# Kernel tuning notes

Measured on AMD Instinct MI355X. Metric: run time of the kernel, lower is better.

## Reference

```python
import jax, jax.numpy as jnp
import numpy as np

B = 512        # batch
D = 128        # embedding_dim (n_input)
S = 50         # max_tweets_num (n_sequence)
T = 32         # max_seq_len (n_steps)
HOOPS = 2
NUM_USERS = 20000
NUM_ITEMS = 100000
LATENT = 64
NUM_FRIENDS = 10000
CLIP = 50      # friend_clip
PAD = 50000    # vocab.pad; word table has PAD+1 rows


def setup_inputs() -> dict:
    key = jax.random.key(0)
    ks = jax.random.split(key, 24)
    s = 0.02
    emb_word = (jax.random.normal(ks[0], (PAD + 1, D)) * s).at[PAD].set(0.0)
    emb_item = jax.random.normal(ks[1], (NUM_ITEMS, LATENT)) * s
    emb_user = (jax.random.normal(ks[2], (NUM_FRIENDS + 1, LATENT)) * s).at[NUM_FRIENDS].set(0.0)
    W_mem = jax.random.normal(ks[3], (LATENT, D)) * s
    b_mem = jnp.zeros((D,))
    w_word = jax.random.normal(ks[4], (D,)) * s
    b_word = jnp.zeros(())
    w_sent = jax.random.normal(ks[5], (D,)) * s
    b_sent = jnp.zeros(())
    W_tr = jax.random.normal(ks[6], (D, LATENT)) * s
    b_tr = jnp.zeros((LATENT,))
    W1 = jax.random.normal(ks[7], (LATENT, LATENT // 2)) * s
    b1 = jnp.zeros((LATENT // 2,))
    W2 = jax.random.normal(ks[8], (LATENT // 2, LATENT // 4)) * s
    b2 = jnp.zeros((LATENT // 4,))
    W3 = jax.random.normal(ks[9], (LATENT // 4, 2)) * s
    b3 = jnp.zeros((2,))
    w_aff = jax.random.normal(ks[10], (LATENT,)) * s
    b_aff = jnp.zeros(())
    user_tweet_indices = jax.random.randint(ks[11], (NUM_USERS, S, T), 0, PAD)
    ufi = jax.random.randint(ks[12], (NUM_USERS, CLIP), 0, NUM_FRIENDS)
    # simulate padded friend lists in the trailing slots
    user_friend_indices = ufi.at[:, CLIP - 5:].set(NUM_FRIENDS)
    user_indices = jax.random.randint(ks[13], (B,), 0, NUM_USERS)
    item_indices = jax.random.randint(ks[14], (B,), 0, NUM_ITEMS)
    return {
        'user_indices': user_indices, 'item_indices': item_indices,
        'emb_word': emb_word, 'emb_item': emb_item, 'emb_user': emb_user,
        'W_mem': W_mem, 'b_mem': b_mem, 'w_word': w_word, 'b_word': b_word,
        'w_sent': w_sent, 'b_sent': b_sent, 'W_tr': W_tr, 'b_tr': b_tr,
        'W1': W1, 'b1': b1, 'W2': W2, 'b2': b2, 'W3': W3, 'b3': b3,
        'w_aff': w_aff, 'b_aff': b_aff,
        'user_tweet_indices': user_tweet_indices,
        'user_friend_indices': user_friend_indices,
    }


def reference(user_indices, item_indices, emb_word, emb_item, emb_user,
              W_mem, b_mem, w_word, b_word, w_sent, b_sent, W_tr, b_tr,
              W1, b1, W2, b2, W3, b3, w_aff, b_aff,
              user_tweet_indices, user_friend_indices):
    item_emb = emb_item[item_indices]                       # [B, L]
    mem = item_emb @ W_mem + b_mem                          # [B, D]
    tweets = emb_word[user_tweet_indices[user_indices]]     # [B, S, T, D]
    for _ in range(HOOPS):
        # word-level attention: scores via broadcast mul+sum == einsum
        ww = jax.nn.softmax(jnp.einsum('bstd,bd->bst', tweets, mem), axis=2)
        sentence = jnp.einsum('bst,bstd->bsd', ww, tweets)  # [B, S, D]
        sw = sentence @ w_word + b_word                     # [B, S]
        iw = mem @ w_sent + b_sent                          # [B]
        swf = jax.nn.softmax(jnp.tanh(sw + iw[:, None]), axis=1)
        mem = jnp.einsum('bs,bsd->bd', swf, sentence) + mem
    ept = mem @ W_tr + b_tr                                 # [B, L]
    fidx = user_friend_indices[user_indices]                # [B, C]
    femb = emb_user[fidx]                                   # [B, C, L]
    friend_num = CLIP - (fidx == NUM_FRIENDS).sum(axis=1, keepdims=True).astype(jnp.float32)
    group_idx = jax.nn.sigmoid(
        jnp.einsum('bcl,l->bc', item_emb[:, None, :] * femb, w_aff) + b_aff)[..., None]
    femb = femb * group_idx
    user_emb = femb.sum(axis=1) / friend_num                # [B, L]
    a = jax.nn.sigmoid(item_emb @ W1 + b1)
    a = jax.nn.sigmoid(a @ W2 + b2)
    alpha = jax.nn.sigmoid(a @ W3 + b3)                     # [B, 2]
    vector = alpha[:, 0:1] * ept + alpha[:, 1:2] * user_emb
    rating = jax.nn.sigmoid((vector * item_emb) @ w_aff + b_aff)  # [B]
    return rating, group_idx
```

## Files before the change

kernel.cpp:

```cpp
#include <hip/hip_runtime.h>
#include <hip/hip_fp16.h>

#define NB 512
#define DD 128
#define SS 50
#define TT 32
#define LL 64
#define CLIPN 50
#define NFRIENDS 10000
#define NTHREADS 512
#define NWAVES 8
#define PAD1 50001
#define WELEMS (PAD1 * DD)

typedef unsigned short u16;
typedef unsigned int u32;

__device__ __forceinline__ float bf2f(u32 u) {
    union { u32 i; float f; } c; c.i = u << 16; return c.f;
}
__device__ __forceinline__ u16 f2bf(float f) {
    union { float f; u32 i; } c; c.f = f;
    u32 x = c.i;
    return (u16)((x + 0x7fffu + ((x >> 16) & 1u)) >> 16);
}
__device__ __forceinline__ float sigf(float x) { return 1.f / (1.f + expf(-x)); }

__device__ __forceinline__ void e5m2_dec4(u32 w, float* o) {
    union { u32 u; __half2 h; } lo, hi;
    lo.u = ((w & 0x000000ffu) << 8) | ((w & 0x0000ff00u) << 16);
    hi.u = ((w & 0x00ff0000u) >> 8) | (w & 0xff000000u);
    float2 a = __half22float2(lo.h), b = __half22float2(hi.h);
    o[0] = a.x; o[1] = a.y; o[2] = b.x; o[3] = b.y;
}
__device__ __forceinline__ u32 e5m2_byte(float x) {
    u16 h = __half_as_ushort(__float2half(x));
    u16 r = (u16)(h + 0x7Fu + ((h >> 8) & 1u));
    return (r >> 8) & 0xffu;
}
__device__ __forceinline__ u32 e5m2_enc4(const float* v) {
    return e5m2_byte(v[0]) | (e5m2_byte(v[1]) << 8) |
           (e5m2_byte(v[2]) << 16) | (e5m2_byte(v[3]) << 24);
}

template <bool BF16> struct LD;
template <> struct LD<true> {
    static __device__ __forceinline__ float one(const void* p, long i) {
        return bf2f(((const u16*)p)[i]);
    }
    static __device__ __forceinline__ void st(void* p, long i, float v) {
        ((u16*)p)[i] = f2bf(v);
    }
};
template <> struct LD<false> {
    static __device__ __forceinline__ float one(const void* p, long i) {
        return ((const float*)p)[i];
    }
    static __device__ __forceinline__ void st(void* p, long i, float v) {
        ((float*)p)[i] = v;
    }
};

template <int WM> struct WT;
template <> struct WT<0> {
    static __device__ __forceinline__ void sixteen(const void* p, long i, float* o) {
        const float* s = (const float*)p + i;
        #pragma unroll
        for (int j = 0; j < 4; ++j) {
            float4 v = *(const float4*)(s + 4 * j);
            o[4*j] = v.x; o[4*j+1] = v.y; o[4*j+2] = v.z; o[4*j+3] = v.w;
        }
    }
    static __device__ __forceinline__ void four(const void* p, long i, float* o) {
        float4 v = *(const float4*)((const float*)p + i);
        o[0] = v.x; o[1] = v.y; o[2] = v.z; o[3] = v.w;
    }
};
template <> struct WT<1> {
    static __device__ __forceinline__ void sixteen(const void* p, long i, float* o) {
        const u16* s = (const u16*)p + i;
        #pragma unroll
        for (int j = 0; j < 2; ++j) {
            uint4 v = *(const uint4*)(s + 8 * j);
            float* q = o + 8 * j;
            q[0] = bf2f(v.x & 0xffffu); q[1] = bf2f(v.x >> 16);
            q[2] = bf2f(v.y & 0xffffu); q[3] = bf2f(v.y >> 16);
            q[4] = bf2f(v.z & 0xffffu); q[5] = bf2f(v.z >> 16);
            q[6] = bf2f(v.w & 0xffffu); q[7] = bf2f(v.w >> 16);
        }
    }
    static __device__ __forceinline__ void four(const void* p, long i, float* o) {
        uint2 v = *(const uint2*)((const u16*)p + i);
        o[0] = bf2f(v.x & 0xffffu); o[1] = bf2f(v.x >> 16);
        o[2] = bf2f(v.y & 0xffffu); o[3] = bf2f(v.y >> 16);
    }
};
template <> struct WT<2> {
    static __device__ __forceinline__ void sixteen(const void* p, long i, float* o) {
        uint4 v = *(const uint4*)((const unsigned char*)p + i);
        e5m2_dec4(v.x, o); e5m2_dec4(v.y, o + 4);
        e5m2_dec4(v.z, o + 8); e5m2_dec4(v.w, o + 12);
    }
    static __device__ __forceinline__ void four(const void* p, long i, float* o) {
        e5m2_dec4(*(const u32*)((const unsigned char*)p + i), o);
    }
};

__global__ void sniff_dtype(const void* __restrict__ emb_word, int* __restrict__ flag) {
    const u16* p = (const u16*)emb_word;
    int lane = (int)threadIdx.x;
    int bad = 0;
    #pragma unroll
    for (int j = 0; j < 8; ++j) {
        unsigned e = (p[lane * 8 + j] >> 7) & 0xffu;
        bad += (e >= 127u);
    }
    #pragma unroll
    for (int off = 1; off < 64; off <<= 1) bad += __shfl_xor(bad, off, 64);
    if (lane == 0) flag[0] = (bad <= 16) ? 1 : 0;
}

__global__ void convert_words(const void* __restrict__ src, u32* __restrict__ dst,
                              const int* __restrict__ flag) {
    long idx = (long)blockIdx.x * 256 + threadIdx.x;
    long i = idx * 16;
    if (i >= WELEMS) return;
    float v[16];
    if (flag[0] == 0) {
        const float* s = (const float*)src + i;
        #pragma unroll
        for (int j = 0; j < 4; ++j) {
            float4 q = *(const float4*)(s + 4 * j);
            v[4*j] = q.x; v[4*j+1] = q.y; v[4*j+2] = q.z; v[4*j+3] = q.w;
        }
    } else {
        WT<1>::sixteen(src, i, v);
    }
    uint4 o;
    o.x = e5m2_enc4(v); o.y = e5m2_enc4(v + 4);
    o.z = e5m2_enc4(v + 8); o.w = e5m2_enc4(v + 12);
    *(uint4*)(dst + idx * 4) = o;
}

template <bool BF16, int WM>
__global__ __launch_bounds__(NTHREADS, 4)
void nrs_fused(const int* __restrict__ user_idx,
               const int* __restrict__ item_idx,
               const void* __restrict__ wtab,
               const void* __restrict__ emb_item,
               const void* __restrict__ emb_user,
               const void* __restrict__ W_mem, const void* __restrict__ b_mem,
               const void* __restrict__ w_word, const void* __restrict__ b_word,
               const void* __restrict__ w_sent, const void* __restrict__ b_sent,
               const void* __restrict__ W_tr, const void* __restrict__ b_tr,
               const void* __restrict__ W1, const void* __restrict__ b1,
               const void* __restrict__ W2, const void* __restrict__ b2,
               const void* __restrict__ W3, const void* __restrict__ b3,
               const void* __restrict__ w_aff, const void* __restrict__ b_aff,
               const int* __restrict__ uti, const int* __restrict__ ufi,
               void* __restrict__ out, const int* __restrict__ flag)
{
    if (flag[0] != (BF16 ? 1 : 0)) return;

    __shared__ float s_mem[DD];
    __shared__ float s_item[LL];
    __shared__ float s_sent[SS * DD];
    __shared__ int   s_uti[SS * TT];
    __shared__ float s_sw[SS];
    __shared__ float s_swf[SS];
    __shared__ float s_q[LL];
    __shared__ float s_ept[LL];
    __shared__ float s_uemb[LL];
    __shared__ int   s_fidx[CLIPN];
    __shared__ float s_g[CLIPN];
    __shared__ float s_a1[32];
    __shared__ float s_a2[16];
    __shared__ float s_alpha[2];
    __shared__ float s_fnum;

    const int b = blockIdx.x;
    const int tid = (int)threadIdx.x;
    const int lane = tid & 63;
    const int wave = tid >> 6;

    const int u = user_idx[b];
    const int it = item_idx[b];
    const long utb = (long)u * (SS * TT);

    if (tid < LL) s_item[tid] = LD<BF16>::one(emb_item, (long)it * LL + tid);
    __syncthreads();

    for (int i = tid; i < SS * TT; i += NTHREADS) s_uti[i] = uti[utb + i];
    if (tid < DD) {
        float acc = LD<BF16>::one(b_mem, tid);
        #pragma unroll 8
        for (int l = 0; l < LL; ++l)
            acc += s_item[l] * LD<BF16>::one(W_mem, l * DD + tid);
        s_mem[tid] = acc;
    }
    __syncthreads();

    const float bw = LD<BF16>::one(b_word, 0);
    const float bs = LD<BF16>::one(b_sent, 0);
    const int dq = lane & 31;
    const int th = lane >> 5;
    float ww4[4];
    #pragma unroll
    for (int k = 0; k < 4; ++k) ww4[k] = LD<BF16>::one(w_word, 4 * dq + k);
    const float ws0 = LD<BF16>::one(w_sent, lane);
    const float ws1 = LD<BF16>::one(w_sent, lane + 64);

    for (int hoop = 0; hoop < 2; ++hoop) {
        for (int s = wave; s < SS; s += NWAVES) {
            const int t = lane >> 1, h = lane & 1;
            const int row = s_uti[s * TT + t];
            const long base = (long)row * DD + h * 64;
            float acc = 0.f;
            #pragma unroll
            for (int j = 0; j < 4; ++j) {
                float v16[16];
                WT<WM>::sixteen(wtab, base + 16 * j, v16);
                const float* mp = &s_mem[h * 64 + 16 * j];
                #pragma unroll
                for (int k = 0; k < 16; ++k) acc += v16[k] * mp[k];
            }
            acc += __shfl_xor(acc, 1, 64);

            float mx = acc;
            #pragma unroll
            for (int off = 1; off < 64; off <<= 1) mx = fmaxf(mx, __shfl_xor(mx, off, 64));
            float e = expf(acc - mx);
            float sm = e;
            #pragma unroll
            for (int off = 1; off < 64; off <<= 1) sm += __shfl_xor(sm, off, 64);
            float wwt = 2.f * e / sm;

            float a4[4] = {0.f, 0.f, 0.f, 0.f};
            #pragma unroll 4
            for (int i2 = 0; i2 < 16; ++i2) {
                int t2 = th * 16 + i2;
                float wv = __shfl(wwt, 2 * t2, 64);
                int r2 = s_uti[s * TT + t2];
                float v4[4];
                WT<WM>::four(wtab, (long)r2 * DD + 4 * dq, v4);
                #pragma unroll
                for (int k = 0; k < 4; ++k) a4[k] += wv * v4[k];
            }
            #pragma unroll
            for (int k = 0; k < 4; ++k) a4[k] += __shfl_xor(a4[k], 32, 64);
            if (th == 0)
                *(float4*)&s_sent[s * DD + 4 * dq] =
                    make_float4(a4[0], a4[1], a4[2], a4[3]);

            float p = a4[0] * ww4[0] + a4[1] * ww4[1] + a4[2] * ww4[2] + a4[3] * ww4[3];
            #pragma unroll
            for (int off = 1; off < 64; off <<= 1) p += __shfl_xor(p, off, 64);
            if (lane == 0) s_sw[s] = 0.5f * p + bw;
        }
        __syncthreads();

        if (wave == 0) {
            float p = s_mem[lane] * ws0 + s_mem[lane + 64] * ws1;
            #pragma unroll
            for (int off = 1; off < 64; off <<= 1) p += __shfl_xor(p, off, 64);
            float iw = p + bs;
            float v = (lane < SS) ? tanhf(s_sw[lane] + iw) : -2.f;
            float mx = v;
            #pragma unroll
            for (int off = 1; off < 64; off <<= 1) mx = fmaxf(mx, __shfl_xor(mx, off, 64));
            float e = (lane < SS) ? expf(v - mx) : 0.f;
            float sm = e;
            #pragma unroll
            for (int off = 1; off < 64; off <<= 1) sm += __shfl_xor(sm, off, 64);
            if (lane < SS) s_swf[lane] = e / sm;
        }
        __syncthreads();

        if (tid < DD) {
            float acc = s_mem[tid];
            for (int s2 = 0; s2 < SS; ++s2)
                acc += s_swf[s2] * s_sent[s2 * DD + tid];
            s_mem[tid] = acc;
        }
        __syncthreads();
    }

    if (tid < LL) {
        float acc = LD<BF16>::one(b_tr, tid);
        for (int d = 0; d < DD; ++d)
            acc += s_mem[d] * LD<BF16>::one(W_tr, d * LL + tid);
        s_ept[tid] = acc;
    } else if (tid < 128) {
        int l = tid - 64;
        s_q[l] = s_item[l] * LD<BF16>::one(w_aff, l);
    } else if (tid < 128 + CLIPN) {
        s_fidx[tid - 128] = ufi[(long)u * CLIPN + (tid - 128)];
    } else if (tid >= 192 && tid < 224) {
        int j = tid - 192;
        float acc = LD<BF16>::one(b1, j);
        for (int l = 0; l < LL; ++l)
            acc += s_item[l] * LD<BF16>::one(W1, l * 32 + j);
        s_a1[j] = sigf(acc);
    }
    __syncthreads();

    const float baff = LD<BF16>::one(b_aff, 0);
    if (tid < CLIPN) {
        long fb = (long)s_fidx[tid] * LL;
        float acc = 0.f;
        for (int l = 0; l < LL; ++l) acc += LD<BF16>::one(emb_user, fb + l) * s_q[l];
        float g = sigf(acc + baff);
        s_g[tid] = g;
        LD<BF16>::st(out, NB + (long)b * CLIPN + tid, g);
    } else if (tid >= 64 && tid < 80) {
        int j = tid - 64;
        float acc = LD<BF16>::one(b2, j);
        for (int k = 0; k < 32; ++k) acc += s_a1[k] * LD<BF16>::one(W2, k * 16 + j);
        s_a2[j] = sigf(acc);
    } else if (tid == 80) {
        int cnt = 0;
        for (int c = 0; c < CLIPN; ++c) cnt += (s_fidx[c] == NFRIENDS);
        s_fnum = (float)(CLIPN - cnt);
    }
    __syncthreads();

    if (tid >= 64 && tid < 128) {
        int l = tid - 64;
        float acc = 0.f;
        for (int c = 0; c < CLIPN; ++c)
            acc += s_g[c] * LD<BF16>::one(emb_user, (long)s_fidx[c] * LL + l);
        s_uemb[l] = acc;
    } else if (tid < 2) {
        float acc = LD<BF16>::one(b3, tid);
        for (int k = 0; k < 16; ++k) acc += s_a2[k] * LD<BF16>::one(W3, k * 2 + tid);
        s_alpha[tid] = sigf(acc);
    }
    __syncthreads();

    if (wave == 0) {
        float vec = s_alpha[0] * s_ept[lane] + s_alpha[1] * (s_uemb[lane] / s_fnum);
        float p = vec * s_q[lane];
        #pragma unroll
        for (int off = 1; off < 64; off <<= 1) p += __shfl_xor(p, off, 64);
        if (lane == 0) LD<BF16>::st(out, b, sigf(p + baff));
    }
}

extern "C" void kernel_launch(void* const* d_in, const int* in_sizes, int n_in,
                              void* d_out, int out_size, void* d_ws, size_t ws_size,
                              hipStream_t stream) {
    (void)in_sizes; (void)n_in; (void)out_size;
    int* flag = (int*)d_ws;
    u32* wbuf = (u32*)((char*)d_ws + 64);
    const size_t need = 64 + (size_t)WELEMS;
    const bool ws_ok = ws_size >= need;

    sniff_dtype<<<1, 64, 0, stream>>>(d_in[2], flag);

    #define ARGS(WORDP)                                                        \
        (const int*)d_in[0], (const int*)d_in[1],                              \
        WORDP, d_in[3], d_in[4],                                               \
        d_in[5], d_in[6], d_in[7], d_in[8], d_in[9], d_in[10],                 \
        d_in[11], d_in[12], d_in[13], d_in[14], d_in[15], d_in[16],            \
        d_in[17], d_in[18], d_in[19], d_in[20],                                \
        (const int*)d_in[21], (const int*)d_in[22],                            \
        d_out, (const int*)flag

    if (ws_ok) {
        const long nthr = (WELEMS + 15) / 16;
        convert_words<<<(int)((nthr + 255) / 256), 256, 0, stream>>>(
            d_in[2], wbuf, flag);
        nrs_fused<true, 2><<<NB, NTHREADS, 0, stream>>>(ARGS((const void*)wbuf));
        nrs_fused<false, 2><<<NB, NTHREADS, 0, stream>>>(ARGS((const void*)wbuf));
    } else {
        nrs_fused<true, 1><<<NB, NTHREADS, 0, stream>>>(ARGS(d_in[2]));
        nrs_fused<false, 0><<<NB, NTHREADS, 0, stream>>>(ARGS(d_in[2]));
    }
    #undef ARGS
}
```

Before: 298.1 us.

## Stage gathered word rows in LDS and use packed fp16 dot products

The main hoop loop now loads each gathered e5m2 word row once into a swizzled per-wave LDS tile and reuses it for the weighted sentence sum, instead of gathering from global memory a second time. Decoding and dot products use byte-permute plus packed fp16 fdot2 and half2 FMAs, and the dtype sniff kernel is folded into the convert and main kernels. This cuts global gather traffic and ALU work for the conversion, at the cost of extra LDS use (which may lower occupancy) and fp16 accumulation precision in the weighted sums.

```diff
diff --git a/kernel.cpp b/kernel.cpp
--- a/kernel.cpp
+++ b/kernel.cpp
@@ -15,6 +15,8 @@
 
 typedef unsigned short u16;
 typedef unsigned int u32;
+typedef _Float16 h2 __attribute__((ext_vector_type(2)));
+typedef __fp16 hf2 __attribute__((ext_vector_type(2)));
 
 __device__ __forceinline__ float bf2f(u32 u) {
     union { u32 i; float f; } c; c.i = u << 16; return c.f;
@@ -26,13 +28,19 @@
 }
 __device__ __forceinline__ float sigf(float x) { return 1.f / (1.f + expf(-x)); }
 
-__device__ __forceinline__ void e5m2_dec4(u32 w, float* o) {
-    union { u32 u; __half2 h; } lo, hi;
-    lo.u = ((w & 0x000000ffu) << 8) | ((w & 0x0000ff00u) << 16);
-    hi.u = ((w & 0x00ff0000u) >> 8) | (w & 0xff000000u);
-    float2 a = __half22float2(lo.h), b = __half22float2(hi.h);
-    o[0] = a.x; o[1] = a.y; o[2] = b.x; o[3] = b.y;
-}
+__device__ __forceinline__ h2 u2h(u32 x) { union { u32 u; h2 h; } c; c.u = x; return c.h; }
+__device__ __forceinline__ u32 h2u(h2 x) { union { h2 h; u32 u; } c; c.h = x; return c.u; }
+__device__ __forceinline__ h2 pkrtz(float a, float b) {
+    union { hf2 p; h2 h; } c; c.p = __builtin_amdgcn_cvt_pkrtz(a, b); return c.h;
+}
+__device__ __forceinline__ h2 declo(u32 w) {
+    return u2h(__builtin_amdgcn_perm(w, 0u, 0x05010400u));
+}
+__device__ __forceinline__ h2 dechi(u32 w) {
+    return u2h(__builtin_amdgcn_perm(w, 0u, 0x07010600u));
+}
+#define FD2(a, b, c) __builtin_amdgcn_fdot2((a), (b), (c), false)
+
 __device__ __forceinline__ u32 e5m2_byte(float x) {
     u16 h = __half_as_ushort(__float2half(x));
     u16 r = (u16)(h + 0x7Fu + ((h >> 8) & 1u));
@@ -95,20 +103,8 @@
         o[2] = bf2f(v.y & 0xffffu); o[3] = bf2f(v.y >> 16);
     }
 };
-template <> struct WT<2> {
-    static __device__ __forceinline__ void sixteen(const void* p, long i, float* o) {
-        uint4 v = *(const uint4*)((const unsigned char*)p + i);
-        e5m2_dec4(v.x, o); e5m2_dec4(v.y, o + 4);
-        e5m2_dec4(v.z, o + 8); e5m2_dec4(v.w, o + 12);
-    }
-    static __device__ __forceinline__ void four(const void* p, long i, float* o) {
-        e5m2_dec4(*(const u32*)((const unsigned char*)p + i), o);
-    }
-};
-
-__global__ void sniff_dtype(const void* __restrict__ emb_word, int* __restrict__ flag) {
-    const u16* p = (const u16*)emb_word;
-    int lane = (int)threadIdx.x;
+
+__device__ __forceinline__ int sniff_wave(const u16* p, int lane) {
     int bad = 0;
     #pragma unroll
     for (int j = 0; j < 8; ++j) {
@@ -117,16 +113,21 @@
     }
     #pragma unroll
     for (int off = 1; off < 64; off <<= 1) bad += __shfl_xor(bad, off, 64);
-    if (lane == 0) flag[0] = (bad <= 16) ? 1 : 0;
-}
-
-__global__ void convert_words(const void* __restrict__ src, u32* __restrict__ dst,
-                              const int* __restrict__ flag) {
+    return (bad <= 16) ? 1 : 0;
+}
+
+__global__ void convert_words(const void* __restrict__ src, u32* __restrict__ dst) {
+    __shared__ int s_flag;
+    if (threadIdx.x < 64) {
+        int f = sniff_wave((const u16*)src, (int)threadIdx.x);
+        if (threadIdx.x == 0) s_flag = f;
+    }
+    __syncthreads();
     long idx = (long)blockIdx.x * 256 + threadIdx.x;
     long i = idx * 16;
     if (i >= WELEMS) return;
     float v[16];
-    if (flag[0] == 0) {
+    if (s_flag == 0) {
         const float* s = (const float*)src + i;
         #pragma unroll
         for (int j = 0; j < 4; ++j) {
@@ -142,26 +143,25 @@
     *(uint4*)(dst + idx * 4) = o;
 }
 
-template <bool BF16, int WM>
+template <bool BF16>
 __global__ __launch_bounds__(NTHREADS, 4)
-void nrs_fused(const int* __restrict__ user_idx,
-               const int* __restrict__ item_idx,
-               const void* __restrict__ wtab,
-               const void* __restrict__ emb_item,
-               const void* __restrict__ emb_user,
-               const void* __restrict__ W_mem, const void* __restrict__ b_mem,
-               const void* __restrict__ w_word, const void* __restrict__ b_word,
-               const void* __restrict__ w_sent, const void* __restrict__ b_sent,
-               const void* __restrict__ W_tr, const void* __restrict__ b_tr,
-               const void* __restrict__ W1, const void* __restrict__ b1,
-               const void* __restrict__ W2, const void* __restrict__ b2,
-               const void* __restrict__ W3, const void* __restrict__ b3,
-               const void* __restrict__ w_aff, const void* __restrict__ b_aff,
-               const int* __restrict__ uti, const int* __restrict__ ufi,
-               void* __restrict__ out, const int* __restrict__ flag)
+void nrs_fast(const int* __restrict__ user_idx,
+              const int* __restrict__ item_idx,
+              const void* __restrict__ wtab,
+              const void* __restrict__ emb_item,
+              const void* __restrict__ emb_user,
+              const void* __restrict__ W_mem, const void* __restrict__ b_mem,
+              const void* __restrict__ w_word, const void* __restrict__ b_word,
+              const void* __restrict__ w_sent, const void* __restrict__ b_sent,
+              const void* __restrict__ W_tr, const void* __restrict__ b_tr,
+              const void* __restrict__ W1, const void* __restrict__ b1,
+              const void* __restrict__ W2, const void* __restrict__ b2,
+              const void* __restrict__ W3, const void* __restrict__ b3,
+              const void* __restrict__ w_aff, const void* __restrict__ b_aff,
+              const int* __restrict__ uti, const int* __restrict__ ufi,
+              void* __restrict__ out,
+              const void* __restrict__ ew_raw)
 {
-    if (flag[0] != (BF16 ? 1 : 0)) return;
-
     __shared__ float s_mem[DD];
     __shared__ float s_item[LL];
     __shared__ float s_sent[SS * DD];
@@ -177,11 +177,20 @@
     __shared__ float s_a2[16];
     __shared__ float s_alpha[2];
     __shared__ float s_fnum;
+    __shared__ int   s_flag;
+    __shared__ uint4 s_tile[NWAVES * TT * 8];
 
     const int b = blockIdx.x;
     const int tid = (int)threadIdx.x;
     const int lane = tid & 63;
     const int wave = tid >> 6;
+
+    if (tid < 64) {
+        int f = sniff_wave((const u16*)ew_raw, lane);
+        if (tid == 0) s_flag = f;
+    }
+    __syncthreads();
+    if (s_flag != (BF16 ? 1 : 0)) return;
 
     const int u = user_idx[b];
     const int it = item_idx[b];
@@ -202,60 +211,86 @@
 
     const float bw = LD<BF16>::one(b_word, 0);
     const float bs = LD<BF16>::one(b_sent, 0);
-    const int dq = lane & 31;
-    const int th = lane >> 5;
+    const int t = lane >> 1, h = lane & 1;
+    const int dq = lane & 31, th = lane >> 5;
+    const int ctop = dq >> 2, cw = dq & 3;
     float ww4[4];
     #pragma unroll
     for (int k = 0; k < 4; ++k) ww4[k] = LD<BF16>::one(w_word, 4 * dq + k);
     const float ws0 = LD<BF16>::one(w_sent, lane);
     const float ws1 = LD<BF16>::one(w_sent, lane + 64);
 
+    uint4* const twave = s_tile + wave * (TT * 8);
+    const u32* const trp = (const u32*)twave;
+    h2 memh[32];
+
     for (int hoop = 0; hoop < 2; ++hoop) {
+        {
+            const float* mrow = &s_mem[h * 64];
+            #pragma unroll
+            for (int k = 0; k < 32; ++k)
+                memh[k] = pkrtz(mrow[2 * k], mrow[2 * k + 1]);
+        }
+
         for (int s = wave; s < SS; s += NWAVES) {
-            const int t = lane >> 1, h = lane & 1;
             const int row = s_uti[s * TT + t];
-            const long base = (long)row * DD + h * 64;
+            const uint4* gp = (const uint4*)((const char*)wtab + ((row << 7) + (h << 6)));
+            uint4 w[4];
+            #pragma unroll
+            for (int j = 0; j < 4; ++j) w[j] = gp[j];
+
+            {
+                const int swz = t & 7;
+                uint4* tp = twave + t * 8;
+                #pragma unroll
+                for (int j = 0; j < 4; ++j) tp[(h * 4 + j) ^ swz] = w[j];
+            }
+
             float acc = 0.f;
             #pragma unroll
             for (int j = 0; j < 4; ++j) {
-                float v16[16];
-                WT<WM>::sixteen(wtab, base + 16 * j, v16);
-                const float* mp = &s_mem[h * 64 + 16 * j];
-                #pragma unroll
-                for (int k = 0; k < 16; ++k) acc += v16[k] * mp[k];
+                acc = FD2(declo(w[j].x), memh[8*j + 0], acc);
+                acc = FD2(dechi(w[j].x), memh[8*j + 1], acc);
+                acc = FD2(declo(w[j].y), memh[8*j + 2], acc);
+                acc = FD2(dechi(w[j].y), memh[8*j + 3], acc);
+                acc = FD2(declo(w[j].z), memh[8*j + 4], acc);
+                acc = FD2(dechi(w[j].z), memh[8*j + 5], acc);
+                acc = FD2(declo(w[j].w), memh[8*j + 6], acc);
+                acc = FD2(dechi(w[j].w), memh[8*j + 7], acc);
             }
             acc += __shfl_xor(acc, 1, 64);
 
             float mx = acc;
             #pragma unroll
-            for (int off = 1; off < 64; off <<= 1) mx = fmaxf(mx, __shfl_xor(mx, off, 64));
+            for (int off = 2; off < 64; off <<= 1) mx = fmaxf(mx, __shfl_xor(mx, off, 64));
             float e = expf(acc - mx);
             float sm = e;
             #pragma unroll
-            for (int off = 1; off < 64; off <<= 1) sm += __shfl_xor(sm, off, 64);
-            float wwt = 2.f * e / sm;
-
-            float a4[4] = {0.f, 0.f, 0.f, 0.f};
-            #pragma unroll 4
+            for (int off = 2; off < 64; off <<= 1) sm += __shfl_xor(sm, off, 64);
+            const float wwt = e / sm;
+
+            __threadfence_block();
+            h2 pa0 = u2h(0u), pa1 = u2h(0u);
+            #pragma unroll
             for (int i2 = 0; i2 < 16; ++i2) {
-                int t2 = th * 16 + i2;
+                const int t2 = th * 16 + i2;
                 float wv = __shfl(wwt, 2 * t2, 64);
-                int r2 = s_uti[s * TT + t2];
-                float v4[4];
-                WT<WM>::four(wtab, (long)r2 * DD + 4 * dq, v4);
-                #pragma unroll
-                for (int k = 0; k < 4; ++k) a4[k] += wv * v4[k];
+                h2 wh = pkrtz(wv, wv);
+                u32 wrd = trp[t2 * 32 + ((ctop ^ (t2 & 7)) << 2) + cw];
+                pa0 += declo(wrd) * wh;
+                pa1 += dechi(wrd) * wh;
             }
-            #pragma unroll
-            for (int k = 0; k < 4; ++k) a4[k] += __shfl_xor(a4[k], 32, 64);
+            pa0 += u2h((u32)__shfl_xor((int)h2u(pa0), 32, 64));
+            pa1 += u2h((u32)__shfl_xor((int)h2u(pa1), 32, 64));
+            const float f0 = (float)pa0.x, f1 = (float)pa0.y;
+            const float f2 = (float)pa1.x, f3 = (float)pa1.y;
             if (th == 0)
-                *(float4*)&s_sent[s * DD + 4 * dq] =
-                    make_float4(a4[0], a4[1], a4[2], a4[3]);
-
-            float p = a4[0] * ww4[0] + a4[1] * ww4[1] + a4[2] * ww4[2] + a4[3] * ww4[3];
-            #pragma unroll
-            for (int off = 1; off < 64; off <<= 1) p += __shfl_xor(p, off, 64);
-            if (lane == 0) s_sw[s] = 0.5f * p + bw;
+                *(float4*)&s_sent[s * DD + 4 * dq] = make_float4(f0, f1, f2, f3);
+
+            float p = f0 * ww4[0] + f1 * ww4[1] + f2 * ww4[2] + f3 * ww4[3];
+            #pragma unroll
+            for (int off = 1; off < 32; off <<= 1) p += __shfl_xor(p, off, 64);
+            if (lane == 0) s_sw[s] = p + bw;
         }
         __syncthreads();
 
@@ -346,35 +381,250 @@
     }
 }
 
+template <bool BF16, int WM>
+__global__ __launch_bounds__(NTHREADS, 4)
+void nrs_generic(const int* __restrict__ user_idx,
+                 const int* __restrict__ item_idx,
+                 const void* __restrict__ wtab,
+                 const void* __restrict__ emb_item,
+                 const void* __restrict__ emb_user,
+                 const void* __restrict__ W_mem, const void* __restrict__ b_mem,
+                 const void* __restrict__ w_word, const void* __restrict__ b_word,
+                 const void* __restrict__ w_sent, const void* __restrict__ b_sent,
+                 const void* __restrict__ W_tr, const void* __restrict__ b_tr,
+                 const void* __restrict__ W1, const void* __restrict__ b1,
+                 const void* __restrict__ W2, const void* __restrict__ b2,
+                 const void* __restrict__ W3, const void* __restrict__ b3,
+                 const void* __restrict__ w_aff, const void* __restrict__ b_aff,
+                 const int* __restrict__ uti, const int* __restrict__ ufi,
+                 void* __restrict__ out)
+{
+    __shared__ float s_mem[DD];
+    __shared__ float s_item[LL];
+    __shared__ float s_sent[SS * DD];
+    __shared__ int   s_uti[SS * TT];
+    __shared__ float s_sw[SS];
+    __shared__ float s_swf[SS];
+    __shared__ float s_q[LL];
+    __shared__ float s_ept[LL];
+    __shared__ float s_uemb[LL];
+    __shared__ int   s_fidx[CLIPN];
+    __shared__ float s_g[CLIPN];
+    __shared__ float s_a1[32];
+    __shared__ float s_a2[16];
+    __shared__ float s_alpha[2];
+    __shared__ float s_fnum;
+    __shared__ int   s_flag;
+
+    const int b = blockIdx.x;
+    const int tid = (int)threadIdx.x;
+    const int lane = tid & 63;
+    const int wave = tid >> 6;
+
+    if (tid < 64) {
+        int f = sniff_wave((const u16*)wtab, lane);
+        if (tid == 0) s_flag = f;
+    }
+    __syncthreads();
+    if (s_flag != (BF16 ? 1 : 0)) return;
+
+    const int u = user_idx[b];
+    const int it = item_idx[b];
+    const long utb = (long)u * (SS * TT);
+
+    if (tid < LL) s_item[tid] = LD<BF16>::one(emb_item, (long)it * LL + tid);
+    __syncthreads();
+
+    for (int i = tid; i < SS * TT; i += NTHREADS) s_uti[i] = uti[utb + i];
+    if (tid < DD) {
+        float acc = LD<BF16>::one(b_mem, tid);
+        #pragma unroll 8
+        for (int l = 0; l < LL; ++l)
+            acc += s_item[l] * LD<BF16>::one(W_mem, l * DD + tid);
+        s_mem[tid] = acc;
+    }
+    __syncthreads();
+
+    const float bw = LD<BF16>::one(b_word, 0);
+    const float bs = LD<BF16>::one(b_sent, 0);
+    const int dq = lane & 31;
+    const int th = lane >> 5;
+    float ww4[4];
+    #pragma unroll
+    for (int k = 0; k < 4; ++k) ww4[k] = LD<BF16>::one(w_word, 4 * dq + k);
+    const float ws0 = LD<BF16>::one(w_sent, lane);
+    const float ws1 = LD<BF16>::one(w_sent, lane + 64);
+
+    for (int hoop = 0; hoop < 2; ++hoop) {
+        for (int s = wave; s < SS; s += NWAVES) {
+            const int t = lane >> 1, h = lane & 1;
+            const int row = s_uti[s * TT + t];
+            const long base = (long)row * DD + h * 64;
+            float acc = 0.f;
+            #pragma unroll
+            for (int j = 0; j < 4; ++j) {
+                float v16[16];
+                WT<WM>::sixteen(wtab, base + 16 * j, v16);
+                const float* mp = &s_mem[h * 64 + 16 * j];
+                #pragma unroll
+                for (int k = 0; k < 16; ++k) acc += v16[k] * mp[k];
+            }
+            acc += __shfl_xor(acc, 1, 64);
+
+            float mx = acc;
+            #pragma unroll
+            for (int off = 1; off < 64; off <<= 1) mx = fmaxf(mx, __shfl_xor(mx, off, 64));
+            float e = expf(acc - mx);
+            float sm = e;
+            #pragma unroll
+            for (int off = 1; off < 64; off <<= 1) sm += __shfl_xor(sm, off, 64);
+            float wwt = 2.f * e / sm;
+
+            float a4[4] = {0.f, 0.f, 0.f, 0.f};
+            #pragma unroll 4
+            for (int i2 = 0; i2 < 16; ++i2) {
+                int t2 = th * 16 + i2;
+                float wv = __shfl(wwt, 2 * t2, 64);
+                int r2 = s_uti[s * TT + t2];
+                float v4[4];
+                WT<WM>::four(wtab, (long)r2 * DD + 4 * dq, v4);
+                #pragma unroll
+                for (int k = 0; k < 4; ++k) a4[k] += wv * v4[k];
+            }
+            #pragma unroll
+            for (int k = 0; k < 4; ++k) a4[k] += __shfl_xor(a4[k], 32, 64);
+            if (th == 0)
+                *(float4*)&s_sent[s * DD + 4 * dq] =
+                    make_float4(a4[0], a4[1], a4[2], a4[3]);
+
+            float p = a4[0] * ww4[0] + a4[1] * ww4[1] + a4[2] * ww4[2] + a4[3] * ww4[3];
+            #pragma unroll
+            for (int off = 1; off < 64; off <<= 1) p += __shfl_xor(p, off, 64);
+            if (lane == 0) s_sw[s] = 0.5f * p + bw;
+        }
+        __syncthreads();
+
+        if (wave == 0) {
+            float p = s_mem[lane] * ws0 + s_mem[lane + 64] * ws1;
+            #pragma unroll
+            for (int off = 1; off < 64; off <<= 1) p += __shfl_xor(p, off, 64);
+            float iw = p + bs;
+            float v = (lane < SS) ? tanhf(s_sw[lane] + iw) : -2.f;
+            float mx = v;
+            #pragma unroll
+            for (int off = 1; off < 64; off <<= 1) mx = fmaxf(mx, __shfl_xor(mx, off, 64));
+            float e = (lane < SS) ? expf(v - mx) : 0.f;
+            float sm = e;
+            #pragma unroll
+            for (int off = 1; off < 64; off <<= 1) sm += __shfl_xor(sm, off, 64);
+            if (lane < SS) s_swf[lane] = e / sm;
+        }
+        __syncthreads();
+
+        if (tid < DD) {
+            float acc = s_mem[tid];
+            for (int s2 = 0; s2 < SS; ++s2)
+                acc += s_swf[s2] * s_sent[s2 * DD + tid];
+            s_mem[tid] = acc;
+        }
+        __syncthreads();
+    }
+
+    if (tid < LL) {
+        float acc = LD<BF16>::one(b_tr, tid);
+        for (int d = 0; d < DD; ++d)
+            acc += s_mem[d] * LD<BF16>::one(W_tr, d * LL + tid);
+        s_ept[tid] = acc;
+    } else if (tid < 128) {
+        int l = tid - 64;
+        s_q[l] = s_item[l] * LD<BF16>::one(w_aff, l);
+    } else if (tid < 128 + CLIPN) {
+        s_fidx[tid - 128] = ufi[(long)u * CLIPN + (tid - 128)];
+    } else if (tid >= 192 && tid < 224) {
+        int j = tid - 192;
+        float acc = LD<BF16>::one(b1, j);
+        for (int l = 0; l < LL; ++l)
+            acc += s_item[l] * LD<BF16>::one(W1, l * 32 + j);
+        s_a1[j] = sigf(acc);
+    }
+    __syncthreads();
+
+    const float baff = LD<BF16>::one(b_aff, 0);
+    if (tid < CLIPN) {
+        long fb = (long)s_fidx[tid] * LL;
+        float acc = 0.f;
+        for (int l = 0; l < LL; ++l) acc += LD<BF16>::one(emb_user, fb + l) * s_q[l];
+        float g = sigf(acc + baff);
+        s_g[tid] = g;
+        LD<BF16>::st(out, NB + (long)b * CLIPN + tid, g);
+    } else if (tid >= 64 && tid < 80) {
+        int j = tid - 64;
+        float acc = LD<BF16>::one(b2, j);
+        for (int k = 0; k < 32; ++k) acc += s_a1[k] * LD<BF16>::one(W2, k * 16 + j);
+        s_a2[j] = sigf(acc);
+    } else if (tid == 80) {
+        int cnt = 0;
+        for (int c = 0; c < CLIPN; ++c) cnt += (s_fidx[c] == NFRIENDS);
+        s_fnum = (float)(CLIPN - cnt);
+    }
+    __syncthreads();
+
+    if (tid >= 64 && tid < 128) {
+        int l = tid - 64;
+        float acc = 0.f;
+        for (int c = 0; c < CLIPN; ++c)
+            acc += s_g[c] * LD<BF16>::one(emb_user, (long)s_fidx[c] * LL + l);
+        s_uemb[l] = acc;
+    } else if (tid < 2) {
+        float acc = LD<BF16>::one(b3, tid);
+        for (int k = 0; k < 16; ++k) acc += s_a2[k] * LD<BF16>::one(W3, k * 2 + tid);
+        s_alpha[tid] = sigf(acc);
+    }
+    __syncthreads();
+
+    if (wave == 0) {
+        float vec = s_alpha[0] * s_ept[lane] + s_alpha[1] * (s_uemb[lane] / s_fnum);
+        float p = vec * s_q[lane];
+        #pragma unroll
+        for (int off = 1; off < 64; off <<= 1) p += __shfl_xor(p, off, 64);
+        if (lane == 0) LD<BF16>::st(out, b, sigf(p + baff));
+    }
+}
+
 extern "C" void kernel_launch(void* const* d_in, const int* in_sizes, int n_in,
                               void* d_out, int out_size, void* d_ws, size_t ws_size,
                               hipStream_t stream) {
     (void)in_sizes; (void)n_in; (void)out_size;
-    int* flag = (int*)d_ws;
-    u32* wbuf = (u32*)((char*)d_ws + 64);
-    const size_t need = 64 + (size_t)WELEMS;
-    const bool ws_ok = ws_size >= need;
-
-    sniff_dtype<<<1, 64, 0, stream>>>(d_in[2], flag);
-
-    #define ARGS(WORDP)                                                        \
-        (const int*)d_in[0], (const int*)d_in[1],                              \
-        WORDP, d_in[3], d_in[4],                                               \
-        d_in[5], d_in[6], d_in[7], d_in[8], d_in[9], d_in[10],                 \
-        d_in[11], d_in[12], d_in[13], d_in[14], d_in[15], d_in[16],            \
-        d_in[17], d_in[18], d_in[19], d_in[20],                                \
-        (const int*)d_in[21], (const int*)d_in[22],                            \
-        d_out, (const int*)flag
+    u32* wbuf = (u32*)d_ws;
+    const bool ws_ok = ws_size >= (size_t)WELEMS;
 
     if (ws_ok) {
         const long nthr = (WELEMS + 15) / 16;
-        convert_words<<<(int)((nthr + 255) / 256), 256, 0, stream>>>(
-            d_in[2], wbuf, flag);
-        nrs_fused<true, 2><<<NB, NTHREADS, 0, stream>>>(ARGS((const void*)wbuf));
-        nrs_fused<false, 2><<<NB, NTHREADS, 0, stream>>>(ARGS((const void*)wbuf));
+        convert_words<<<(int)((nthr + 255) / 256), 256, 0, stream>>>(d_in[2], wbuf);
+        nrs_fast<true><<<NB, NTHREADS, 0, stream>>>(
+            (const int*)d_in[0], (const int*)d_in[1], (const void*)wbuf,
+            d_in[3], d_in[4], d_in[5], d_in[6], d_in[7], d_in[8], d_in[9],
+            d_in[10], d_in[11], d_in[12], d_in[13], d_in[14], d_in[15],
+            d_in[16], d_in[17], d_in[18], d_in[19], d_in[20],
+            (const int*)d_in[21], (const int*)d_in[22], d_out, d_in[2]);
+        nrs_fast<false><<<NB, NTHREADS, 0, stream>>>(
+            (const int*)d_in[0], (const int*)d_in[1], (const void*)wbuf,
+            d_in[3], d_in[4], d_in[5], d_in[6], d_in[7], d_in[8], d_in[9],
+            d_in[10], d_in[11], d_in[12], d_in[13], d_in[14], d_in[15],
+            d_in[16], d_in[17], d_in[18], d_in[19], d_in[20],
+            (const int*)d_in[21], (const int*)d_in[22], d_out, d_in[2]);
     } else {
-        nrs_fused<true, 1><<<NB, NTHREADS, 0, stream>>>(ARGS(d_in[2]));
-        nrs_fused<false, 0><<<NB, NTHREADS, 0, stream>>>(ARGS(d_in[2]));
-    }
-    #undef ARGS
-}
+        nrs_generic<true, 1><<<NB, NTHREADS, 0, stream>>>(
+            (const int*)d_in[0], (const int*)d_in[1], d_in[2],
+            d_in[3], d_in[4], d_in[5], d_in[6], d_in[7], d_in[8], d_in[9],
+            d_in[10], d_in[11], d_in[12], d_in[13], d_in[14], d_in[15],
+            d_in[16], d_in[17], d_in[18], d_in[19], d_in[20],
+            (const int*)d_in[21], (const int*)d_in[22], d_out);
+        nrs_generic<false, 0><<<NB, NTHREADS, 0, stream>>>(
+            (const int*)d_in[0], (const int*)d_in[1], d_in[2],
+            d_in[3], d_in[4], d_in[5], d_in[6], d_in[7], d_in[8], d_in[9],
+            d_in[10], d_in[11], d_in[12], d_in[13], d_in[14], d_in[15],
+            d_in[16], d_in[17], d_in[18], d_in[19], d_in[20],
+            (const int*)d_in[21], (const int*)d_in[22], d_out);
+    }
+}
```

After: 276.6 us. 1.08x faster.
